# Optimization experiments

Measured on AMD Instinct MI355X. Metric: run time of the kernel, lower is better.

Reference implementation:

```python
import jax, jax.numpy as jnp
import numpy as np

B, S, E = 2, 2048, 2048
H, KV, D = 32, 8, 128
EPS = 1e-6


def _rope_tables(seq_len, head_dim, base=1_000_000.0):
    inv_freq = 1.0 / (base ** (np.arange(0, head_dim, 2, dtype=np.float32) / head_dim))
    ang = np.arange(seq_len, dtype=np.float32)[:, None] * inv_freq[None, :]  # [S, D/2]
    cos = np.concatenate([np.cos(ang), np.cos(ang)], axis=-1)  # [S, D]
    sin = np.concatenate([np.sin(ang), np.sin(ang)], axis=-1)
    return jnp.asarray(cos), jnp.asarray(sin)


def setup_inputs() -> dict:
    key = jax.random.key(0)
    ks = jax.random.split(key, 8)
    x = jax.random.normal(ks[0], (B, S, E), dtype=jnp.float32)
    mask = jnp.triu(jnp.ones((S, S), dtype=bool), k=1)  # True = masked (causal)
    cos, sin = _rope_tables(S, D)
    w = 0.02
    Wq = jax.random.normal(ks[1], (E, H * D), dtype=jnp.float32) * w
    bq = jnp.zeros((H * D,), dtype=jnp.float32)
    Wk = jax.random.normal(ks[2], (E, KV * D), dtype=jnp.float32) * w
    bk = jnp.zeros((KV * D,), dtype=jnp.float32)
    Wv = jax.random.normal(ks[3], (E, KV * D), dtype=jnp.float32) * w
    bv = jnp.zeros((KV * D,), dtype=jnp.float32)
    Wo = jax.random.normal(ks[4], (H * D, E), dtype=jnp.float32) * w
    q_scale = jnp.ones((D,), dtype=jnp.float32)
    k_scale = jnp.ones((D,), dtype=jnp.float32)
    return {"x": x, "mask": mask, "cos": cos, "sin": sin, "Wq": Wq, "bq": bq,
            "Wk": Wk, "bk": bk, "Wv": Wv, "bv": bv, "Wo": Wo,
            "q_scale": q_scale, "k_scale": k_scale}


def _rmsnorm(x, scale):
    xf = x.astype(jnp.float32)
    var = jnp.mean(xf * xf, axis=-1, keepdims=True)
    return (xf * jax.lax.rsqrt(var + EPS) * scale).astype(x.dtype)


def _apply_rope(x, cos, sin):
    # x: [B, h, S, D]; cos/sin: [S, D]
    d2 = x.shape[-1] // 2
    x1, x2 = x[..., :d2], x[..., d2:]
    rotated = jnp.concatenate([-x2, x1], axis=-1)
    return (x * cos[None, None] + rotated * sin[None, None]).astype(x.dtype)


def reference(x, mask, cos, sin, Wq, bq, Wk, bk, Wv, bv, Wo, q_scale, k_scale):
    b, s, _ = x.shape
    q = (x @ Wq + bq).reshape(b, s, H, D).transpose(0, 2, 1, 3)   # [B,H,S,D]
    k = (x @ Wk + bk).reshape(b, s, KV, D).transpose(0, 2, 1, 3)  # [B,KV,S,D]
    v = (x @ Wv + bv).reshape(b, s, KV, D).transpose(0, 2, 1, 3)
    q = _rmsnorm(q, q_scale)
    k = _rmsnorm(k, k_scale)
    q = _apply_rope(q, cos, sin)
    k = _apply_rope(k, cos, sin)
    group = H // KV
    k = jnp.repeat(k, group, axis=1)  # repeat_interleave on head dim -> [B,H,S,D]
    v = jnp.repeat(v, group, axis=1)
    scores = jnp.einsum("bhqd,bhkd->bhqk", q, k)
    scores = jnp.where(mask[None, None], -jnp.inf, scores)
    attn = jax.nn.softmax(scores / jnp.sqrt(jnp.float32(D)), axis=-1)
    ctx = jnp.einsum("bhqk,bhkd->bhqd", attn, v)
    ctx = ctx.transpose(0, 2, 1, 3).reshape(b, s, H * D)
    return ctx @ Wo
```

## Files before the change

kernel.cpp:

```cpp
#include <hip/hip_runtime.h>

typedef short short8 __attribute__((ext_vector_type(8)));
typedef float f32x4 __attribute__((ext_vector_type(4)));
typedef float f32x16 __attribute__((ext_vector_type(16)));
typedef unsigned int uint2v __attribute__((ext_vector_type(2)));

static __device__ __forceinline__ ushort f2bf(float f){
  union { float f; uint u; } cv; cv.f = f;
  uint u = cv.u;
  uint r = (u + 0x7fffu + ((u >> 16) & 1u)) >> 16;
  return (ushort)r;
}
static __device__ __forceinline__ float bf2f(ushort h){
  union { uint u; float f; } cv; cv.u = ((uint)h) << 16; return cv.f;
}
static __device__ __forceinline__ f32x4 mfma16x16x32(short8 a, short8 b, f32x4 c){
  return __builtin_amdgcn_mfma_f32_16x16x32_bf16(a, b, c, 0, 0, 0);
}
static __device__ __forceinline__ f32x16 mfma32(short8 a, short8 b, f32x16 c){
  return __builtin_amdgcn_mfma_f32_32x32x16_bf16(a, b, c, 0, 0, 0);
}
static __device__ __forceinline__ float ex2(float x){
  float r; asm("v_exp_f32 %0, %1" : "=v"(r) : "v"(x)); return r;
}
static __device__ __forceinline__ uint cvtpk(float lo, float hi){
  uint r; asm("v_cvt_pk_bf16_f32 %0, %1, %2" : "=v"(r) : "v"(lo), "v"(hi)); return r;
}
static __device__ __forceinline__ void glds16(const void* g, const void* l){
  __builtin_amdgcn_global_load_lds((const __attribute__((address_space(1))) void*)g,
                                   (__attribute__((address_space(3))) void*)l, 16, 0, 0);
}
static __device__ __forceinline__ void store_out(float* p, float v){ *p = v; }
static __device__ __forceinline__ void store_out(ushort* p, float v){ *p = f2bf(v); }
static __device__ __forceinline__ int xcd_swizzle(int flat, int nwg){
  int q = nwg >> 3, r = nwg & 7;
  int xcd = flat & 7, idx = flat >> 3;
  return (xcd < r) ? xcd * (q + 1) + idx : r * (q + 1) + (xcd - r) * q + idx;
}

__global__ void cvt_bf16_kernel(const float* __restrict__ x, ushort* __restrict__ y, int n4){
  int i = blockIdx.x * 256 + threadIdx.x;
  if (i < n4){
    float4 v = reinterpret_cast<const float4*>(x)[i];
    ushort4 o; o.x = f2bf(v.x); o.y = f2bf(v.y); o.z = f2bf(v.z); o.w = f2bf(v.w);
    reinterpret_cast<ushort4*>(y)[i] = o;
  }
}

__global__ void transpose_cvt_kernel(const float* __restrict__ W, ushort* __restrict__ WT, int K, int N){
  __shared__ float tile[32][33];
  int n0 = blockIdx.x * 32, k0 = blockIdx.y * 32;
  int tx = threadIdx.x, ty = threadIdx.y;
  #pragma unroll
  for (int i = 0; i < 4; i++){ int r = ty + i * 8; tile[r][tx] = W[(size_t)(k0 + r) * N + n0 + tx]; }
  __syncthreads();
  #pragma unroll
  for (int i = 0; i < 4; i++){ int r = ty + i * 8; WT[(size_t)(n0 + r) * K + k0 + tx] = f2bf(tile[tx][r]); }
}

__global__ void bias_concat_kernel(const float* __restrict__ bq, const float* __restrict__ bk,
                                   const float* __restrict__ bv, float* __restrict__ out){
  int i = blockIdx.x * 256 + threadIdx.x;
  if (i < 6144) out[i] = (i < 4096) ? bq[i] : ((i < 5120) ? bk[i - 4096] : bv[i - 5120]);
}

template<typename OutT>
__global__ __launch_bounds__(256) void gemm_bt_kernel(const ushort* __restrict__ A, const ushort* __restrict__ BT,
                                                      const float* __restrict__ bias, OutT* __restrict__ C,
                                                      int M, int N, int K){
  __shared__ ushort As[128 * 32];
  __shared__ ushort Bs[128 * 32];
  const int nwg = gridDim.x * gridDim.y;
  const int wg = xcd_swizzle(blockIdx.y * gridDim.x + blockIdx.x, nwg);
  const int m0 = (wg / gridDim.x) * 128, n0 = (wg % gridDim.x) * 128;
  const int tid = threadIdx.x, w = tid >> 6, l = tid & 63, lm = l & 15, lk = l >> 4;
  const int wr = w >> 1, wc = w & 1;
  const int srow0 = (w * 64 + l) >> 2, srow1 = 64 + srow0;
  const int sseg  = l & 3;
  const int sw0 = sseg ^ ((srow0 >> 1) & 3), sw1 = sseg ^ ((srow1 >> 1) & 3);
  const int rchunk = lk ^ ((lm >> 1) & 3);
  const size_t aoff0 = (size_t)(m0 + srow0) * K + sw0 * 8;
  const size_t aoff1 = (size_t)(m0 + srow1) * K + sw1 * 8;
  const size_t boff0 = (size_t)(n0 + srow0) * K + sw0 * 8;
  const size_t boff1 = (size_t)(n0 + srow1) * K + sw1 * 8;
  ushort* dstA0 = &As[(w * 64) * 8];
  ushort* dstA1 = &As[(256 + w * 64) * 8];
  ushort* dstB0 = &Bs[(w * 64) * 8];
  ushort* dstB1 = &Bs[(256 + w * 64) * 8];
  f32x4 acc[4][4] = {};
  for (int k0 = 0; k0 < K; k0 += 32){
    __syncthreads();
    glds16(A  + aoff0 + k0, dstA0);
    glds16(A  + aoff1 + k0, dstA1);
    glds16(BT + boff0 + k0, dstB0);
    glds16(BT + boff1 + k0, dstB1);
    __syncthreads();
    short8 af[4], bfr[4];
    #pragma unroll
    for (int mi = 0; mi < 4; mi++) af[mi]  = *(const short8*)&As[(wr * 64 + mi * 16 + lm) * 32 + rchunk * 8];
    #pragma unroll
    for (int ni = 0; ni < 4; ni++) bfr[ni] = *(const short8*)&Bs[(wc * 64 + ni * 16 + lm) * 32 + rchunk * 8];
    #pragma unroll
    for (int mi = 0; mi < 4; mi++)
      #pragma unroll
      for (int ni = 0; ni < 4; ni++)
        acc[mi][ni] = mfma16x16x32(af[mi], bfr[ni], acc[mi][ni]);
  }
  #pragma unroll
  for (int mi = 0; mi < 4; mi++)
    #pragma unroll
    for (int ni = 0; ni < 4; ni++){
      int col = n0 + wc * 64 + ni * 16 + lm;
      float bb = bias ? bias[col] : 0.0f;
      #pragma unroll
      for (int r = 0; r < 4; r++){
        int row = m0 + wr * 64 + mi * 16 + lk * 4 + r;
        store_out(&C[(size_t)row * N + col], acc[mi][ni][r] + bb);
      }
    }
}

#define QSCL2 0.12752016f
__global__ __launch_bounds__(256) void norm_rope_kernel(const ushort* __restrict__ qkv,
    const float* __restrict__ cosT, const float* __restrict__ sinT,
    const float* __restrict__ qs, const float* __restrict__ ksc,
    ushort* __restrict__ qo, ushort* __restrict__ ko, ushort* __restrict__ vto){
  int slot = blockIdx.x * 4 + (threadIdx.x >> 6);
  int lane = threadIdx.x & 63;
  int row = slot / 48, c = slot % 48;
  int b = row >> 11, s = row & 2047;
  size_t base = (size_t)row * 6144 + c * 128;
  float e1 = bf2f(qkv[base + lane]);
  float e2 = bf2f(qkv[base + lane + 64]);
  if (c < 40){
    float ss = e1 * e1 + e2 * e2;
    #pragma unroll
    for (int m = 1; m < 64; m <<= 1) ss += __shfl_xor(ss, m);
    float rs = rsqrtf(ss * (1.0f / 128.0f) + 1e-6f);
    const float* sc = (c < 32) ? qs : ksc;
    float n1 = e1 * rs * sc[lane], n2 = e2 * rs * sc[lane + 64];
    float c1 = cosT[s * 128 + lane],      s1 = sinT[s * 128 + lane];
    float c2 = cosT[s * 128 + lane + 64], s2 = sinT[s * 128 + lane + 64];
    float o1 = n1 * c1 - n2 * s1;
    float o2 = n2 * c2 + n1 * s2;
    if (c < 32){
      size_t ob = ((size_t)(b * 32 + c) * 2048 + s) * 128;
      qo[ob + lane] = f2bf(o1 * QSCL2); qo[ob + lane + 64] = f2bf(o2 * QSCL2);
    } else {
      int kv = c - 32;
      size_t ob = ((size_t)(b * 8 + kv) * 2048 + s) * 128;
      ko[ob + lane] = f2bf(o1); ko[ob + lane + 64] = f2bf(o2);
    }
  } else {
    int kv = c - 40;
    size_t ob = (size_t)(b * 8 + kv) * 128;
    vto[(ob + lane) * 2048 + s]      = f2bf(e1);
    vto[(ob + lane + 64) * 2048 + s] = f2bf(e2);
  }
}

__global__ __launch_bounds__(256, 2) void flash_kernel(const ushort* __restrict__ Q, const ushort* __restrict__ Kg,
    const ushort* __restrict__ VTg, ushort* __restrict__ ctx){
  __shared__ ushort Kl[2][64 * 128];
  __shared__ ushort Vl[2][128 * 64];
  const int bh = blockIdx.y, b = bh >> 5, h = bh & 31, kvh = h >> 2;
  const int bx = blockIdx.x;
  const int tid = threadIdx.x, w = tid >> 6, l = tid & 63;
  const int q31 = l & 31, hi = l >> 5, swz = q31 & 7;
  const ushort* Kbase = Kg  + (size_t)(b * 8 + kvh) * 2048 * 128;
  const ushort* Vbase = VTg + (size_t)(b * 8 + kvh) * 128 * 2048;
  const int krow = l >> 4, kcol = l & 15;
  const int vrow = l >> 3, vcol = l & 7;

  #define STAGE(KT, BS) do {                                                            \
    _Pragma("unroll")                                                                   \
    for (int i2 = 0; i2 < 4; i2++){                                                     \
      int i = w * 4 + i2; int row = i * 4 + krow;                                       \
      glds16(Kbase + (size_t)((KT) * 64 + row) * 128 + ((kcol ^ (row & 7)) * 8),        \
             &Kl[BS][i * 512]);                                                         \
    }                                                                                   \
    _Pragma("unroll")                                                                   \
    for (int j2 = 0; j2 < 4; j2++){                                                     \
      int j = w * 4 + j2; int row = j * 8 + vrow;                                       \
      glds16(Vbase + (size_t)row * 2048 + (KT) * 64 + ((vcol ^ (row & 7)) * 8),         \
             &Vl[BS][j * 512]);                                                         \
    }                                                                                   \
  } while (0)

  for (int pass = 0; pass < 2; pass++){
    const int qb = pass ? bx : (15 - bx);
    const int q0 = qb * 128;
    const int qw = q0 + w * 32;
    const int myq = qw + q31;
    const ushort* Qp = Q + ((size_t)(b * 32 + h) * 2048 + myq) * 128;
    short8 qf[8];
    #pragma unroll
    for (int s = 0; s < 8; s++) qf[s] = *(const short8*)(Qp + s * 16 + hi * 8);
    f32x16 o[4] = {};
    float m_r = -INFINITY, l_r = 0.f;
    const int nt = 2 * qb + 2;

    STAGE(0, 0);
    for (int kt = 0; kt < nt; kt++){
      const int cur = kt & 1;
      if (kt + 1 < nt){
        STAGE(kt + 1, cur ^ 1);
        asm volatile("s_waitcnt vmcnt(8)" ::: "memory");
      } else {
        asm volatile("s_waitcnt vmcnt(0)" ::: "memory");
      }
      __builtin_amdgcn_s_barrier();
      asm volatile("" ::: "memory");
      f32x16 sa0 = {}, sa1 = {};
      __builtin_amdgcn_s_setprio(1);
      #pragma unroll
      for (int s = 0; s < 8; s++){
        short8 a0 = *(const short8*)&Kl[cur][q31 * 128 + (((2 * s + hi) ^ swz) * 8)];
        short8 a1 = *(const short8*)&Kl[cur][(32 + q31) * 128 + (((2 * s + hi) ^ swz) * 8)];
        sa0 = mfma32(a0, qf[s], sa0);
        sa1 = mfma32(a1, qf[s], sa1);
      }
      __builtin_amdgcn_s_setprio(0);
      if (kt >= 2 * qb){
        #pragma unroll
        for (int r = 0; r < 16; r++){
          int krel = (r & 3) + 8 * (r >> 2) + 4 * hi;
          if (kt * 64 + krel > myq)      sa0[r] = -INFINITY;
          if (kt * 64 + 32 + krel > myq) sa1[r] = -INFINITY;
        }
      }
      float mx = fmaxf(sa0[0], sa1[0]);
      #pragma unroll
      for (int r = 1; r < 16; r++) mx = fmaxf(mx, fmaxf(sa0[r], sa1[r]));
      mx = fmaxf(mx, __shfl_xor(mx, 32));
      if (!__all(mx - m_r <= 8.f)){
        float mn = fmaxf(m_r, mx);
        float al = ex2(m_r - mn);
        m_r = mn; l_r *= al;
        #pragma unroll
        for (int r = 0; r < 16; r++){
          float alq = __shfl(al, (r & 3) + 8 * (r >> 2) + 4 * hi);
          o[0][r] *= alq; o[1][r] *= alq; o[2][r] *= alq; o[3][r] *= alq;
        }
      }
      float rsum = 0.f;
      #pragma unroll
      for (int r = 0; r < 16; r++){
        sa0[r] = ex2(sa0[r] - m_r);
        sa1[r] = ex2(sa1[r] - m_r);
        rsum += sa0[r] + sa1[r];
      }
      rsum += __shfl_xor(rsum, 32);
      l_r += rsum;
      uint pk0[8], pk1[8];
      #pragma unroll
      for (int t = 0; t < 8; t++){
        pk0[t] = cvtpk(sa0[2 * t], sa0[2 * t + 1]);
        pk1[t] = cvtpk(sa1[2 * t], sa1[2 * t + 1]);
      }
      __builtin_amdgcn_s_setprio(1);
      #pragma unroll
      for (int sub = 0; sub < 2; sub++){
        #pragma unroll
        for (int kc = 0; kc < 2; kc++){
          uint p0 = sub ? pk1[4 * kc]     : pk0[4 * kc];
          uint p1 = sub ? pk1[4 * kc + 1] : pk0[4 * kc + 1];
          uint p2 = sub ? pk1[4 * kc + 2] : pk0[4 * kc + 2];
          uint p3 = sub ? pk1[4 * kc + 3] : pk0[4 * kc + 3];
          uint2v r02 = __builtin_amdgcn_permlane32_swap(p0, p2, false, false);
          uint2v r13 = __builtin_amdgcn_permlane32_swap(p1, p3, false, false);
          union { uint u[4]; short8 v; } Af;
          Af.u[0] = r02[0]; Af.u[1] = r13[0]; Af.u[2] = r02[1]; Af.u[3] = r13[1];
          #pragma unroll
          for (int dc = 0; dc < 4; dc++){
            short8 vf = *(const short8*)&Vl[cur][(dc * 32 + q31) * 64 + (((4 * sub + 2 * kc + hi) ^ swz) * 8)];
            o[dc] = mfma32(Af.v, vf, o[dc]);
          }
        }
      }
      __builtin_amdgcn_s_setprio(0);
      asm volatile("" ::: "memory");
      __builtin_amdgcn_s_barrier();
    }
    float invl = 1.0f / l_r;
    ushort* Cp = ctx + (size_t)(b * 2048 + qw) * 4096 + (size_t)h * 128;
    #pragma unroll
    for (int r = 0; r < 16; r++){
      int qrel = (r & 3) + 8 * (r >> 2) + 4 * hi;
      float inv = __shfl(invl, qrel);
      #pragma unroll
      for (int dc = 0; dc < 4; dc++)
        Cp[(size_t)qrel * 4096 + dc * 32 + q31] = f2bf(o[dc][r] * inv);
    }
  }
  #undef STAGE
}

extern "C" void kernel_launch(void* const* d_in, const int* in_sizes, int n_in,
                              void* d_out, int out_size, void* d_ws, size_t ws_size,
                              hipStream_t stream){
  const float* x    = (const float*)d_in[0];
  const float* cosT = (const float*)d_in[2];
  const float* sinT = (const float*)d_in[3];
  const float* Wq   = (const float*)d_in[4];
  const float* bq   = (const float*)d_in[5];
  const float* Wk   = (const float*)d_in[6];
  const float* bk   = (const float*)d_in[7];
  const float* Wv   = (const float*)d_in[8];
  const float* bv   = (const float*)d_in[9];
  const float* Wo   = (const float*)d_in[10];
  const float* qs   = (const float*)d_in[11];
  const float* ksc  = (const float*)d_in[12];
  float* out = (float*)d_out;
  char* ws = (char*)d_ws;

  ushort* xb    = (ushort*)(ws + 0);
  ushort* wtqkv = (ushort*)(ws + 16777216);
  float*  biasq = (float* )(ws + 41943040);
  ushort* qkv   = (ushort*)(ws + 41967616);
  ushort* qb_   = (ushort*)(ws + 92299264);
  ushort* kb_   = (ushort*)(ws + 125853696);
  ushort* vtb   = (ushort*)(ws + 134242304);
  ushort* ctx   = (ushort*)(ws + 142630912);
  ushort* wot   = (ushort*)(ws + 176185344);

  cvt_bf16_kernel<<<8192, 256, 0, stream>>>(x, xb, 2097152);
  transpose_cvt_kernel<<<dim3(128, 64), dim3(32, 8), 0, stream>>>(Wq, wtqkv, 2048, 4096);
  transpose_cvt_kernel<<<dim3(32, 64),  dim3(32, 8), 0, stream>>>(Wk, wtqkv + (size_t)4096 * 2048, 2048, 1024);
  transpose_cvt_kernel<<<dim3(32, 64),  dim3(32, 8), 0, stream>>>(Wv, wtqkv + (size_t)5120 * 2048, 2048, 1024);
  transpose_cvt_kernel<<<dim3(64, 128), dim3(32, 8), 0, stream>>>(Wo, wot, 4096, 2048);
  bias_concat_kernel<<<24, 256, 0, stream>>>(bq, bk, bv, biasq);

  gemm_bt_kernel<ushort><<<dim3(48, 32), 256, 0, stream>>>(xb, wtqkv, biasq, qkv, 4096, 6144, 2048);
  norm_rope_kernel<<<49152, 256, 0, stream>>>(qkv, cosT, sinT, qs, ksc, qb_, kb_, vtb);
  flash_kernel<<<dim3(8, 64), 256, 0, stream>>>(qb_, kb_, vtb, ctx);
  gemm_bt_kernel<float><<<dim3(16, 32), 256, 0, stream>>>(ctx, wot, nullptr, out, 4096, 2048, 4096);
}
```

Measured before the change: 418.6 us.

## Replace 128x128 GEMM with double-buffered 256x256 tile, 512-thread kernel

Both projection GEMMs now use a 256x256 output tile computed by 8 waves, with BK=64 staging into double-buffered LDS. Global-to-LDS loads for the next K tile are issued during the MFMA phases of the current tile, and s_setprio is raised around the MFMAs. The larger tile raises arithmetic intensity and hides load latency, where the old kernel loaded and computed with two barriers per K step. In exchange it needs 128KB of LDS per block and more accumulator registers, and the output GEMM launches only 128 blocks, which may leave compute units idle.

```diff
diff --git a/kernel.cpp b/kernel.cpp
--- a/kernel.cpp
+++ b/kernel.cpp
@@ -65,56 +65,88 @@
 }
 
 template<typename OutT>
-__global__ __launch_bounds__(256) void gemm_bt_kernel(const ushort* __restrict__ A, const ushort* __restrict__ BT,
-                                                      const float* __restrict__ bias, OutT* __restrict__ C,
-                                                      int M, int N, int K){
-  __shared__ ushort As[128 * 32];
-  __shared__ ushort Bs[128 * 32];
-  const int nwg = gridDim.x * gridDim.y;
-  const int wg = xcd_swizzle(blockIdx.y * gridDim.x + blockIdx.x, nwg);
-  const int m0 = (wg / gridDim.x) * 128, n0 = (wg % gridDim.x) * 128;
+__global__ __launch_bounds__(512, 2) void gemm256_kernel(const ushort* __restrict__ A, const ushort* __restrict__ BT,
+                                                         const float* __restrict__ bias, OutT* __restrict__ C,
+                                                         int M, int N, int K){
+  __shared__ __align__(16) ushort lds[2][2][2][128 * 64];
+  const int nbx = N >> 8;
+  const int nwg = nbx * (M >> 8);
+  const int wg = xcd_swizzle(blockIdx.x, nwg);
+  const int m0 = (wg / nbx) * 256, n0 = (wg % nbx) * 256;
   const int tid = threadIdx.x, w = tid >> 6, l = tid & 63, lm = l & 15, lk = l >> 4;
-  const int wr = w >> 1, wc = w & 1;
-  const int srow0 = (w * 64 + l) >> 2, srow1 = 64 + srow0;
-  const int sseg  = l & 3;
-  const int sw0 = sseg ^ ((srow0 >> 1) & 3), sw1 = sseg ^ ((srow1 >> 1) & 3);
-  const int rchunk = lk ^ ((lm >> 1) & 3);
-  const size_t aoff0 = (size_t)(m0 + srow0) * K + sw0 * 8;
-  const size_t aoff1 = (size_t)(m0 + srow1) * K + sw1 * 8;
-  const size_t boff0 = (size_t)(n0 + srow0) * K + sw0 * 8;
-  const size_t boff1 = (size_t)(n0 + srow1) * K + sw1 * 8;
-  ushort* dstA0 = &As[(w * 64) * 8];
-  ushort* dstA1 = &As[(256 + w * 64) * 8];
-  ushort* dstB0 = &Bs[(w * 64) * 8];
-  ushort* dstB1 = &Bs[(256 + w * 64) * 8];
-  f32x4 acc[4][4] = {};
-  for (int k0 = 0; k0 < K; k0 += 32){
-    __syncthreads();
-    glds16(A  + aoff0 + k0, dstA0);
-    glds16(A  + aoff1 + k0, dstA1);
-    glds16(BT + boff0 + k0, dstB0);
-    glds16(BT + boff1 + k0, dstB1);
-    __syncthreads();
-    short8 af[4], bfr[4];
-    #pragma unroll
-    for (int mi = 0; mi < 4; mi++) af[mi]  = *(const short8*)&As[(wr * 64 + mi * 16 + lm) * 32 + rchunk * 8];
-    #pragma unroll
-    for (int ni = 0; ni < 4; ni++) bfr[ni] = *(const short8*)&Bs[(wc * 64 + ni * 16 + lm) * 32 + rchunk * 8];
-    #pragma unroll
-    for (int mi = 0; mi < 4; mi++)
-      #pragma unroll
-      for (int ni = 0; ni < 4; ni++)
-        acc[mi][ni] = mfma16x16x32(af[mi], bfr[ni], acc[mi][ni]);
+  const int wr = w >> 2, wc = w & 3;
+  const int sr0 = tid >> 3, sr1 = 64 + sr0, sc = tid & 7;
+  const int scs0 = sc ^ (sr0 & 7), scs1 = sc ^ (sr1 & 7);
+  const int swz = lm & 7;
+
+#define STG_HALF(MAT, H, TK, BUF) do{                                                     \
+    const ushort* _s = (MAT) ? BT : A;                                                    \
+    const int _rb = ((MAT) ? n0 : m0) + (H) * 128;                                        \
+    glds16(_s + (size_t)(_rb + sr0) * K + (size_t)(TK) * 64 + scs0 * 8,                   \
+           &lds[BUF][MAT][H][w * 512]);                                                   \
+    glds16(_s + (size_t)(_rb + sr1) * K + (size_t)(TK) * 64 + scs1 * 8,                   \
+           &lds[BUF][MAT][H][4096 + w * 512]);                                            \
+  }while(0)
+
+#define PHASE(BUF, MQ, NQ, STAGE_CODE) do{                                                \
+    short8 af[4][2], bf[2][2];                                                            \
+    _Pragma("unroll")                                                                     \
+    for (int mi = 0; mi < 4; mi++)                                                        \
+      _Pragma("unroll")                                                                   \
+      for (int ks = 0; ks < 2; ks++)                                                      \
+        af[mi][ks] = *(const short8*)&lds[BUF][0][wr]                                     \
+            [((MQ) * 64 + mi * 16 + lm) * 64 + (((ks * 4 + lk) ^ swz) * 8)];              \
+    _Pragma("unroll")                                                                     \
+    for (int ni = 0; ni < 2; ni++)                                                        \
+      _Pragma("unroll")                                                                   \
+      for (int ks = 0; ks < 2; ks++)                                                      \
+        bf[ni][ks] = *(const short8*)&lds[BUF][1][wc >> 1]                                \
+            [((wc & 1) * 64 + (NQ) * 32 + ni * 16 + lm) * 64 + (((ks * 4 + lk) ^ swz) * 8)]; \
+    STAGE_CODE                                                                            \
+    __builtin_amdgcn_s_barrier();                                                         \
+    __builtin_amdgcn_s_setprio(1);                                                        \
+    _Pragma("unroll")                                                                     \
+    for (int mi = 0; mi < 4; mi++)                                                        \
+      _Pragma("unroll")                                                                   \
+      for (int ni = 0; ni < 2; ni++)                                                      \
+        _Pragma("unroll")                                                                 \
+        for (int ks = 0; ks < 2; ks++)                                                    \
+          acc[(MQ) * 4 + mi][(NQ) * 2 + ni] =                                             \
+              mfma16x16x32(af[mi][ks], bf[ni][ks], acc[(MQ) * 4 + mi][(NQ) * 2 + ni]);    \
+    __builtin_amdgcn_s_setprio(0);                                                        \
+    __builtin_amdgcn_s_barrier();                                                         \
+  }while(0)
+
+  f32x4 acc[8][4] = {};
+  const int J = K >> 7;
+  STG_HALF(0, 0, 0, 0); STG_HALF(0, 1, 0, 0); STG_HALF(1, 0, 0, 0); STG_HALF(1, 1, 0, 0);
+  for (int j = 0; j < J; j++){
+    const int t1 = 2 * j + 1, t2 = 2 * j + 2;
+    const bool last = (j == J - 1);
+    asm volatile("s_waitcnt vmcnt(0)" ::: "memory");
+    __builtin_amdgcn_s_barrier();
+    PHASE(0, 0, 0, { STG_HALF(0, 0, t1, 1); STG_HALF(0, 1, t1, 1); });
+    PHASE(0, 0, 1, { STG_HALF(1, 0, t1, 1); STG_HALF(1, 1, t1, 1); });
+    PHASE(0, 1, 0, {});
+    PHASE(0, 1, 1, {});
+    asm volatile("s_waitcnt vmcnt(0)" ::: "memory");
+    __builtin_amdgcn_s_barrier();
+    PHASE(1, 0, 0, { if (!last){ STG_HALF(0, 0, t2, 0); STG_HALF(0, 1, t2, 0); } });
+    PHASE(1, 0, 1, { if (!last){ STG_HALF(1, 0, t2, 0); STG_HALF(1, 1, t2, 0); } });
+    PHASE(1, 1, 0, {});
+    PHASE(1, 1, 1, {});
   }
+#undef PHASE
+#undef STG_HALF
   #pragma unroll
-  for (int mi = 0; mi < 4; mi++)
+  for (int mi = 0; mi < 8; mi++)
     #pragma unroll
     for (int ni = 0; ni < 4; ni++){
       int col = n0 + wc * 64 + ni * 16 + lm;
       float bb = bias ? bias[col] : 0.0f;
       #pragma unroll
       for (int r = 0; r < 4; r++){
-        int row = m0 + wr * 64 + mi * 16 + lk * 4 + r;
+        int row = m0 + wr * 128 + mi * 16 + lk * 4 + r;
         store_out(&C[(size_t)row * N + col], acc[mi][ni][r] + bb);
       }
     }
@@ -331,8 +363,8 @@
   transpose_cvt_kernel<<<dim3(64, 128), dim3(32, 8), 0, stream>>>(Wo, wot, 4096, 2048);
   bias_concat_kernel<<<24, 256, 0, stream>>>(bq, bk, bv, biasq);
 
-  gemm_bt_kernel<ushort><<<dim3(48, 32), 256, 0, stream>>>(xb, wtqkv, biasq, qkv, 4096, 6144, 2048);
+  gemm256_kernel<ushort><<<384, 512, 0, stream>>>(xb, wtqkv, biasq, qkv, 4096, 6144, 2048);
   norm_rope_kernel<<<49152, 256, 0, stream>>>(qkv, cosT, sinT, qs, ksc, qb_, kb_, vtb);
   flash_kernel<<<dim3(8, 64), 256, 0, stream>>>(qb_, kb_, vtb, ctx);
-  gemm_bt_kernel<float><<<dim3(16, 32), 256, 0, stream>>>(ctx, wot, nullptr, out, 4096, 2048, 4096);
-}
+  gemm256_kernel<float><<<128, 512, 0, stream>>>(ctx, wot, nullptr, out, 4096, 2048, 4096);
+}
```

Result: slower. 432.7 us (+3.4%).

## Rewrite GEMM as 128x256 tile, 512-thread kernel with double-buffered async loads

Applied to the files above, without the earlier changes.

Replaces the 128x128, 256-thread GEMM with a 128x256-tile, 8-wave kernel that uses a K-step of 64 and double-buffers LDS. Global-to-LDS loads for tile t+2 are issued while tile t is computed, with vmcnt waits in place of a full sync. An XOR swizzle avoids LDS bank conflicts, and s_setprio raises wave priority around the MFMA block. The goal is to hide memory latency and raise arithmetic intensity. In exchange, LDS use grows to 96KB per block and the grid gets smaller (256 blocks for the output projection), which may reduce occupancy and leave CUs underused.

```diff
diff --git a/kernel.cpp b/kernel.cpp
--- a/kernel.cpp
+++ b/kernel.cpp
@@ -65,47 +65,67 @@
 }
 
 template<typename OutT>
-__global__ __launch_bounds__(256) void gemm_bt_kernel(const ushort* __restrict__ A, const ushort* __restrict__ BT,
-                                                      const float* __restrict__ bias, OutT* __restrict__ C,
-                                                      int M, int N, int K){
-  __shared__ ushort As[128 * 32];
-  __shared__ ushort Bs[128 * 32];
-  const int nwg = gridDim.x * gridDim.y;
-  const int wg = xcd_swizzle(blockIdx.y * gridDim.x + blockIdx.x, nwg);
-  const int m0 = (wg / gridDim.x) * 128, n0 = (wg % gridDim.x) * 128;
+__global__ __launch_bounds__(512, 2) void gemm256_kernel(const ushort* __restrict__ A, const ushort* __restrict__ BT,
+                                                         const float* __restrict__ bias, OutT* __restrict__ C,
+                                                         int M, int N, int K){
+  __shared__ __align__(16) ushort As[2][128 * 64];
+  __shared__ __align__(16) ushort Bs[2][256 * 64];
+  const int nbx = N >> 8;
+  const int nwg = nbx * (M >> 7);
+  const int wg = xcd_swizzle(blockIdx.x, nwg);
+  const int m0 = (wg / nbx) * 128, n0 = (wg % nbx) * 256;
   const int tid = threadIdx.x, w = tid >> 6, l = tid & 63, lm = l & 15, lk = l >> 4;
-  const int wr = w >> 1, wc = w & 1;
-  const int srow0 = (w * 64 + l) >> 2, srow1 = 64 + srow0;
-  const int sseg  = l & 3;
-  const int sw0 = sseg ^ ((srow0 >> 1) & 3), sw1 = sseg ^ ((srow1 >> 1) & 3);
-  const int rchunk = lk ^ ((lm >> 1) & 3);
-  const size_t aoff0 = (size_t)(m0 + srow0) * K + sw0 * 8;
-  const size_t aoff1 = (size_t)(m0 + srow1) * K + sw1 * 8;
-  const size_t boff0 = (size_t)(n0 + srow0) * K + sw0 * 8;
-  const size_t boff1 = (size_t)(n0 + srow1) * K + sw1 * 8;
-  ushort* dstA0 = &As[(w * 64) * 8];
-  ushort* dstA1 = &As[(256 + w * 64) * 8];
-  ushort* dstB0 = &Bs[(w * 64) * 8];
-  ushort* dstB1 = &Bs[(256 + w * 64) * 8];
+  const int wr = w >> 2, wc = w & 3;
+  const int sr = tid >> 3, sc = tid & 7;
+  const int scs = sc ^ (sr & 7);
+  const int swz = lm & 7;
+  const int nt = K >> 6;
+
+#define STAGE_G(T, BUF) do{                                                                \
+    _Pragma("unroll")                                                                      \
+    for (int r = 0; r < 2; r++)                                                            \
+      glds16(A + (size_t)(m0 + r * 64 + sr) * K + (size_t)(T) * 64 + scs * 8,              \
+             &As[BUF][r * 4096 + w * 512]);                                                \
+    _Pragma("unroll")                                                                      \
+    for (int r = 0; r < 4; r++)                                                            \
+      glds16(BT + (size_t)(n0 + r * 64 + sr) * K + (size_t)(T) * 64 + scs * 8,             \
+             &Bs[BUF][r * 4096 + w * 512]);                                                \
+  }while(0)
+
   f32x4 acc[4][4] = {};
-  for (int k0 = 0; k0 < K; k0 += 32){
-    __syncthreads();
-    glds16(A  + aoff0 + k0, dstA0);
-    glds16(A  + aoff1 + k0, dstA1);
-    glds16(BT + boff0 + k0, dstB0);
-    glds16(BT + boff1 + k0, dstB1);
-    __syncthreads();
-    short8 af[4], bfr[4];
-    #pragma unroll
-    for (int mi = 0; mi < 4; mi++) af[mi]  = *(const short8*)&As[(wr * 64 + mi * 16 + lm) * 32 + rchunk * 8];
-    #pragma unroll
-    for (int ni = 0; ni < 4; ni++) bfr[ni] = *(const short8*)&Bs[(wc * 64 + ni * 16 + lm) * 32 + rchunk * 8];
+  STAGE_G(0, 0);
+  STAGE_G(1, 1);
+  for (int t = 0; t < nt; t++){
+    const int cur = t & 1;
+    if (t < nt - 1) asm volatile("s_waitcnt vmcnt(6)" ::: "memory");
+    else            asm volatile("s_waitcnt vmcnt(0)" ::: "memory");
+    __builtin_amdgcn_s_barrier();
+    asm volatile("" ::: "memory");
+    short8 af[4][2], bf[4][2];
     #pragma unroll
     for (int mi = 0; mi < 4; mi++)
       #pragma unroll
+      for (int ks = 0; ks < 2; ks++)
+        af[mi][ks] = *(const short8*)&As[cur][(wr * 64 + mi * 16 + lm) * 64 + (((ks * 4 + lk) ^ swz) * 8)];
+    #pragma unroll
+    for (int ni = 0; ni < 4; ni++)
+      #pragma unroll
+      for (int ks = 0; ks < 2; ks++)
+        bf[ni][ks] = *(const short8*)&Bs[cur][(wc * 64 + ni * 16 + lm) * 64 + (((ks * 4 + lk) ^ swz) * 8)];
+    __builtin_amdgcn_s_setprio(1);
+    #pragma unroll
+    for (int mi = 0; mi < 4; mi++)
+      #pragma unroll
       for (int ni = 0; ni < 4; ni++)
-        acc[mi][ni] = mfma16x16x32(af[mi], bfr[ni], acc[mi][ni]);
+        #pragma unroll
+        for (int ks = 0; ks < 2; ks++)
+          acc[mi][ni] = mfma16x16x32(af[mi][ks], bf[ni][ks], acc[mi][ni]);
+    __builtin_amdgcn_s_setprio(0);
+    asm volatile("" ::: "memory");
+    __builtin_amdgcn_s_barrier();
+    if (t + 2 < nt) STAGE_G(t + 2, cur);
   }
+#undef STAGE_G
   #pragma unroll
   for (int mi = 0; mi < 4; mi++)
     #pragma unroll
@@ -331,8 +351,8 @@
   transpose_cvt_kernel<<<dim3(64, 128), dim3(32, 8), 0, stream>>>(Wo, wot, 4096, 2048);
   bias_concat_kernel<<<24, 256, 0, stream>>>(bq, bk, bv, biasq);
 
-  gemm_bt_kernel<ushort><<<dim3(48, 32), 256, 0, stream>>>(xb, wtqkv, biasq, qkv, 4096, 6144, 2048);
+  gemm256_kernel<ushort><<<768, 512, 0, stream>>>(xb, wtqkv, biasq, qkv, 4096, 6144, 2048);
   norm_rope_kernel<<<49152, 256, 0, stream>>>(qkv, cosT, sinT, qs, ksc, qb_, kb_, vtb);
   flash_kernel<<<dim3(8, 64), 256, 0, stream>>>(qb_, kb_, vtb, ctx);
-  gemm_bt_kernel<float><<<dim3(16, 32), 256, 0, stream>>>(ctx, wot, nullptr, out, 4096, 2048, 4096);
-}
+  gemm256_kernel<float><<<256, 512, 0, stream>>>(ctx, wot, nullptr, out, 4096, 2048, 4096);
+}
```

Result: faster. 403.1 us (-3.7%).
